# Kernel tuning notes

Measured on AMD Instinct MI355X. Metric: run time of the kernel, lower is better.

The kernel has to match this reference:

```python
import jax, jax.numpy as jnp
import numpy as np

D_MODEL = 1024
N_HEADS = 16
HEAD_DIM = D_MODEL // N_HEADS


def setup_inputs() -> dict:
    key = jax.random.key(0)
    k1, k2, k3 = jax.random.split(key, 3)
    x = jax.random.normal(k1, (4, 2048, D_MODEL), dtype=jnp.float32)
    # torch nn.Linear(d_model, 3*d_model, bias=False): weight [3C, C], y = x @ W.T
    w_qkv = jax.random.normal(k2, (3 * D_MODEL, D_MODEL), dtype=jnp.float32) * (1.0 / np.sqrt(D_MODEL))
    w_out = jax.random.normal(k3, (D_MODEL, D_MODEL), dtype=jnp.float32) * (1.0 / np.sqrt(D_MODEL))
    return {"x": x, "w_qkv": w_qkv, "w_out": w_out}


def reference(x, w_qkv, w_out):
    B, T, C = x.shape
    H, Dh = N_HEADS, HEAD_DIM
    scale = 1.0 / np.sqrt(Dh).astype(np.float32)
    qkv = x @ w_qkv.T  # [B, T, 3C]
    q, k, v = jnp.split(qkv, 3, axis=-1)

    def heads(t):  # [B,T,C] -> [B,H,T,Dh]
        return t.reshape(B, T, H, Dh).transpose(0, 2, 1, 3)

    q, k, v = heads(q), heads(k), heads(v)
    attn = jnp.einsum('bhqd,bhkd->bhqk', q, k) * scale  # [B,H,T,T]
    attn = jax.nn.softmax(attn, axis=-1)
    out = jnp.einsum('bhqk,bhkd->bhqd', attn, v)  # [B,H,T,Dh]
    out = out.transpose(0, 2, 1, 3).reshape(B, T, C)
    return out @ w_out.T
```

## Files before the change

### kernel.cpp

```cpp
#include <hip/hip_runtime.h>
#include <hip/hip_bf16.h>

#define DEVINL __device__ __forceinline__

typedef short s16x8 __attribute__((ext_vector_type(8)));
typedef float f32x4 __attribute__((ext_vector_type(4)));

static constexpr int TC = 1024;
static constexpr int NH = 16;
static constexpr int DH = 64;
static constexpr int TT = 2048;
static constexpr int NB = 4;
static constexpr int MROWS = NB * TT;

static constexpr float QSCALE = 0.18033688011112042f;

DEVINL ushort f32_to_bf16u(float f) {
  uint u = __builtin_bit_cast(uint, f);
  u += 0x7fffu + ((u >> 16) & 1u);
  return (ushort)(u >> 16);
}

DEVINL f32x4 mfma32(s16x8 a, s16x8 b, f32x4 c) {
  return __builtin_amdgcn_mfma_f32_16x16x32_bf16(a, b, c, 0, 0, 0);
}

DEVINL void gload_lds16(const void* g, void* l) {
  __builtin_amdgcn_global_load_lds((const __attribute__((address_space(1))) void*)g,
                                   (__attribute__((address_space(3))) void*)l, 16, 0, 0);
}

DEVINL s16x8 ld8(const ushort* p) { return *reinterpret_cast<const s16x8*>(p); }

DEVINL void cvt_range(const float* __restrict__ src, ushort* __restrict__ dst, int n4,
                      int i0, int stride) {
  for (int i = i0; i < n4; i += stride) {
    float4 v = reinterpret_cast<const float4*>(src)[i];
    ushort4 o;
    o.x = f32_to_bf16u(v.x);
    o.y = f32_to_bf16u(v.y);
    o.z = f32_to_bf16u(v.z);
    o.w = f32_to_bf16u(v.w);
    reinterpret_cast<ushort4*>(dst)[i] = o;
  }
}

__global__ void cvt3_kernel(const float* __restrict__ s0, ushort* __restrict__ d0, int n0,
                            const float* __restrict__ s1, ushort* __restrict__ d1, int n1,
                            const float* __restrict__ s2, ushort* __restrict__ d2, int n2) {
  const int i0 = blockIdx.x * blockDim.x + threadIdx.x;
  const int stride = gridDim.x * blockDim.x;
  cvt_range(s0, d0, n0, i0, stride);
  cvt_range(s1, d1, n1, i0, stride);
  cvt_range(s2, d2, n2, i0, stride);
}

template <int MODE>
__global__ __launch_bounds__(256, 2) void gemm_bt(
    const ushort* __restrict__ A, const ushort* __restrict__ Bw, float* __restrict__ Cout,
    ushort* __restrict__ Qo, ushort* __restrict__ Ko, ushort* __restrict__ Vo, int N) {
  __shared__ __align__(16) ushort As[128 * 64];
  __shared__ __align__(16) ushort Bs[128 * 64];
  const int lane = threadIdx.x & 63;
  const int wid = threadIdx.x >> 6;
  const int bx = blockIdx.x, by = blockIdx.y;
  const int wrow = (wid >> 1) * 64, wcol = (wid & 1) * 64;
  const int lr = lane >> 3;
  const int lc = lane & 7;

  f32x4 acc[4][4] = {};

  for (int kt = 0; kt < TC; kt += 64) {
#pragma unroll
    for (int j = 0; j < 4; ++j) {
      const int seg = wid * 4 + j;
      const int r = seg * 8 + lr;
      const int csrc = lc ^ (r & 7);
      const ushort* ga = A + (size_t)(by * 128 + r) * TC + kt + csrc * 8;
      gload_lds16(ga, &As[seg * 512]);
      const ushort* gb = Bw + (size_t)(bx * 128 + r) * TC + kt + csrc * 8;
      gload_lds16(gb, &Bs[seg * 512]);
    }
    __syncthreads();
#pragma unroll
    for (int kk = 0; kk < 2; ++kk) {
      s16x8 af[4], bfr[4];
#pragma unroll
      for (int m = 0; m < 4; ++m) {
        const int r = wrow + m * 16 + (lane & 15);
        const int ch = (kk * 4 + (lane >> 4)) ^ (r & 7);
        af[m] = *reinterpret_cast<const s16x8*>(&As[r * 64 + ch * 8]);
      }
#pragma unroll
      for (int n = 0; n < 4; ++n) {
        const int r = wcol + n * 16 + (lane & 15);
        const int ch = (kk * 4 + (lane >> 4)) ^ (r & 7);
        bfr[n] = *reinterpret_cast<const s16x8*>(&Bs[r * 64 + ch * 8]);
      }
#pragma unroll
      for (int m = 0; m < 4; ++m)
#pragma unroll
        for (int n = 0; n < 4; ++n) acc[m][n] = mfma32(af[m], bfr[n], acc[m][n]);
    }
    __syncthreads();
  }

#pragma unroll
  for (int m = 0; m < 4; ++m) {
#pragma unroll
    for (int n = 0; n < 4; ++n) {
      const int ng = bx * 128 + wcol + n * 16 + (lane & 15);
      const int mg0 = by * 128 + wrow + m * 16 + (lane >> 4) * 4;
      if (MODE == 0) {
#pragma unroll
        for (int i = 0; i < 4; ++i) Cout[(size_t)(mg0 + i) * N + ng] = acc[m][n][i];
      } else {
        const int sec = ng >> 10;
        const int w = ng & 1023;
        const int h = w >> 6, d = w & 63;
#pragma unroll
        for (int i = 0; i < 4; ++i) {
          const int mg = mg0 + i;
          const int t = mg & (TT - 1);
          const int b = mg >> 11;
          const int bh = b * NH + h;
          const float v = acc[m][n][i];
          if (sec == 0)
            Qo[((size_t)bh * TT + t) * DH + d] = f32_to_bf16u(v * QSCALE);
          else if (sec == 1)
            Ko[((size_t)bh * TT + t) * DH + d] = f32_to_bf16u(v);
          else
            Vo[((size_t)bh * DH + d) * TT + t] = f32_to_bf16u(v);
        }
      }
    }
  }
}

__global__ __launch_bounds__(256, 4) void attn_kernel(const ushort* __restrict__ Q,
                                                      const ushort* __restrict__ K,
                                                      const ushort* __restrict__ V,
                                                      ushort* __restrict__ O) {
  __shared__ __align__(16) ushort Ks[2][64 * 64];
  __shared__ __align__(16) ushort Vs[2][64 * 64];
  const int tid = threadIdx.x;
  const int lane = tid & 63, wid = tid >> 6;
  const int bh = blockIdx.x;
  const int q0 = blockIdx.y * 128 + wid * 32;
  const int qr = lane & 15, lg = lane >> 4;

  const ushort* Qh = Q + (size_t)bh * TT * DH;
  const ushort* Kh = K + (size_t)bh * TT * DH;
  const ushort* Vh = V + (size_t)bh * DH * TT;

  s16x8 qf[2][2];
#pragma unroll
  for (int qt = 0; qt < 2; ++qt)
#pragma unroll
    for (int h = 0; h < 2; ++h)
      qf[qt][h] = ld8(&Qh[(q0 + qt * 16 + qr) * DH + h * 32 + lg * 8]);

  const int pk = 8 * (qr >> 2) + (qr & 3);

  const uint one_bf = 0x3F803F80u;
  const s16x8 ONES = __builtin_bit_cast(s16x8, (uint4){one_bf, one_bf, one_bf, one_bf});

  f32x4 acc[2][4] = {};
  f32x4 acc1[2] = {};

#define SWZ(r) ((r ^ ((r & 8) >> 1)) & 7)

#define STAGE(buf, k0)                                                              \
  {                                                                                 \
    _Pragma("unroll") for (int j = 0; j < 2; ++j) {                                 \
      const int l = tid + 256 * j;                                                  \
      const int row = l >> 3, ch = l & 7;                                           \
      const int sc = ch ^ SWZ(row);                                                 \
      gload_lds16(&Kh[(size_t)((k0) + row) * DH + sc * 8],                          \
                  &Ks[buf][(wid * 64 + 256 * j) * 8]);                              \
      gload_lds16(&Vh[(size_t)row * TT + (k0) + sc * 8],                            \
                  &Vs[buf][(wid * 64 + 256 * j) * 8]);                              \
    }                                                                               \
  }

  STAGE(0, 0);
  __syncthreads();

  for (int t = 0; t < TT / 64; ++t) {
    const int buf = t & 1;
    if (t + 1 < TT / 64) STAGE(buf ^ 1, (t + 1) * 64);
    const ushort* Kb = Ks[buf];
    const ushort* Vb = Vs[buf];

#pragma unroll
    for (int kh = 0; kh < 2; ++kh) {
      s16x8 kf[2][2];
#pragma unroll
      for (int jj = 0; jj < 2; ++jj)
#pragma unroll
        for (int h = 0; h < 2; ++h) {
          const int r = kh * 32 + pk + 4 * jj;
          const int ch = (h * 4 + lg) ^ SWZ(r);
          kf[jj][h] = ld8(&Kb[r * 64 + ch * 8]);
        }
      s16x8 vf[4];
#pragma unroll
      for (int g = 0; g < 4; ++g) {
        const int r = g * 16 + qr;
        const int ch = (kh * 4 + lg) ^ SWZ(r);
        vf[g] = ld8(&Vb[r * 64 + ch * 8]);
      }

#pragma unroll
      for (int qt = 0; qt < 2; ++qt) {
        const f32x4 z = {};
        f32x4 slo = mfma32(kf[0][0], qf[qt][0], z);
        slo = mfma32(kf[0][1], qf[qt][1], slo);
        f32x4 shi = mfma32(kf[1][0], qf[qt][0], z);
        shi = mfma32(kf[1][1], qf[qt][1], shi);

        float p[8];
#pragma unroll
        for (int i = 0; i < 4; ++i) {
          p[i] = __builtin_amdgcn_exp2f(slo[i]);
          p[4 + i] = __builtin_amdgcn_exp2f(shi[i]);
        }

        uint u[4];
#pragma unroll
        for (int e = 0; e < 4; ++e) {
          const uint a0 = __builtin_bit_cast(uint, p[2 * e]) + 0x8000u;
          const uint a1 = __builtin_bit_cast(uint, p[2 * e + 1]) + 0x8000u;
          u[e] = __builtin_amdgcn_perm(a1, a0, 0x07060302u);
        }
        const s16x8 pa = __builtin_bit_cast(s16x8, u);

#pragma unroll
        for (int g = 0; g < 4; ++g) acc[qt][g] = mfma32(pa, vf[g], acc[qt][g]);
        acc1[qt] = mfma32(pa, ONES, acc1[qt]);
      }
    }
    __syncthreads();
  }

  const int b = bh >> 4, h = bh & 15;
#pragma unroll
  for (int qt = 0; qt < 2; ++qt) {
    float inv[4];
#pragma unroll
    for (int i = 0; i < 4; ++i) inv[i] = 1.0f / acc1[qt][i];
#pragma unroll
    for (int g = 0; g < 4; ++g) {
#pragma unroll
      for (int i = 0; i < 4; ++i) {
        const int tq = q0 + qt * 16 + lg * 4 + i;
        const int col = h * DH + g * 16 + qr;
        O[((size_t)b * TT + tq) * TC + col] = f32_to_bf16u(acc[qt][g][i] * inv[i]);
      }
    }
  }
#undef STAGE
#undef SWZ
}

extern "C" void kernel_launch(void* const* d_in, const int* in_sizes, int n_in,
                              void* d_out, int out_size, void* d_ws, size_t ws_size,
                              hipStream_t stream) {
  const float* x = (const float*)d_in[0];
  const float* wqkv = (const float*)d_in[1];
  const float* wout = (const float*)d_in[2];
  float* out = (float*)d_out;
  char* ws = (char*)d_ws;

  ushort* xb    = (ushort*)(ws);
  ushort* wqkvb = (ushort*)(ws + ((size_t)16 << 20));
  ushort* woutb = (ushort*)(ws + ((size_t)22 << 20));
  ushort* qb    = (ushort*)(ws + ((size_t)24 << 20));
  ushort* kb    = (ushort*)(ws + ((size_t)40 << 20));
  ushort* vtb   = (ushort*)(ws + ((size_t)56 << 20));

  cvt3_kernel<<<2048, 256, 0, stream>>>(x, xb, MROWS * TC / 4,
                                        wqkv, wqkvb, 3 * TC * TC / 4,
                                        wout, woutb, TC * TC / 4);

  gemm_bt<1><<<dim3(3 * TC / 128, MROWS / 128), 256, 0, stream>>>(
      xb, wqkvb, nullptr, qb, kb, vtb, 3 * TC);

  attn_kernel<<<dim3(NB * NH, TT / 128), 256, 0, stream>>>(qb, kb, vtb, xb);

  gemm_bt<0><<<dim3(TC / 128, MROWS / 128), 256, 0, stream>>>(
      xb, woutb, out, nullptr, nullptr, nullptr, TC);
}
```

Before: 195.0 us.

## Double-buffer GEMM LDS tiles, swizzle block order, precompute attention LDS offsets

The projection GEMM now double-buffers its A/B shared-memory tiles, so the next K slice loads while MFMAs run on the current one. It also remaps workgroup IDs in an 8-way interleave to improve L2 locality. The attention kernel precomputes its swizzled LDS offsets outside the loop and wraps its MFMA groups in s_setprio to favour matrix issue. Doubling LDS to 64KB per GEMM block may limit the two-blocks-per-CU occupancy the launch bounds request.

```diff
diff --git a/kernel.cpp b/kernel.cpp
--- a/kernel.cpp
+++ b/kernel.cpp
@@ -59,29 +59,43 @@
 __global__ __launch_bounds__(256, 2) void gemm_bt(
     const ushort* __restrict__ A, const ushort* __restrict__ Bw, float* __restrict__ Cout,
     ushort* __restrict__ Qo, ushort* __restrict__ Ko, ushort* __restrict__ Vo, int N) {
-  __shared__ __align__(16) ushort As[128 * 64];
-  __shared__ __align__(16) ushort Bs[128 * 64];
+  __shared__ __align__(16) ushort As[2][128 * 64];
+  __shared__ __align__(16) ushort Bs[2][128 * 64];
   const int lane = threadIdx.x & 63;
   const int wid = threadIdx.x >> 6;
-  const int bx = blockIdx.x, by = blockIdx.y;
+
+  const int nx = gridDim.x;
+  const int nwg = nx * gridDim.y;
+  const int orig = blockIdx.x + nx * blockIdx.y;
+  const int cpx = nwg >> 3;
+  const int swz = (orig & 7) * cpx + (orig >> 3);
+  const int bx = swz % nx, by = swz / nx;
+
   const int wrow = (wid >> 1) * 64, wcol = (wid & 1) * 64;
   const int lr = lane >> 3;
   const int lc = lane & 7;
 
   f32x4 acc[4][4] = {};
 
-  for (int kt = 0; kt < TC; kt += 64) {
-#pragma unroll
-    for (int j = 0; j < 4; ++j) {
-      const int seg = wid * 4 + j;
-      const int r = seg * 8 + lr;
-      const int csrc = lc ^ (r & 7);
-      const ushort* ga = A + (size_t)(by * 128 + r) * TC + kt + csrc * 8;
-      gload_lds16(ga, &As[seg * 512]);
-      const ushort* gb = Bw + (size_t)(bx * 128 + r) * TC + kt + csrc * 8;
-      gload_lds16(gb, &Bs[seg * 512]);
-    }
-    __syncthreads();
+#define GSTAGE(buf, kt)                                                         \
+  {                                                                             \
+    _Pragma("unroll") for (int j = 0; j < 4; ++j) {                             \
+      const int seg = wid * 4 + j;                                              \
+      const int r = seg * 8 + lr;                                               \
+      const int csrc = lc ^ (r & 7);                                            \
+      gload_lds16(A + (size_t)(by * 128 + r) * TC + (kt) + csrc * 8,            \
+                  &As[buf][seg * 512]);                                         \
+      gload_lds16(Bw + (size_t)(bx * 128 + r) * TC + (kt) + csrc * 8,           \
+                  &Bs[buf][seg * 512]);                                         \
+    }                                                                           \
+  }
+
+  GSTAGE(0, 0);
+  __syncthreads();
+
+  for (int t = 0; t < TC / 64; ++t) {
+    const int buf = t & 1;
+    if (t + 1 < TC / 64) GSTAGE(buf ^ 1, (t + 1) * 64);
 #pragma unroll
     for (int kk = 0; kk < 2; ++kk) {
       s16x8 af[4], bfr[4];
@@ -89,13 +103,13 @@
       for (int m = 0; m < 4; ++m) {
         const int r = wrow + m * 16 + (lane & 15);
         const int ch = (kk * 4 + (lane >> 4)) ^ (r & 7);
-        af[m] = *reinterpret_cast<const s16x8*>(&As[r * 64 + ch * 8]);
+        af[m] = ld8(&As[buf][r * 64 + ch * 8]);
       }
 #pragma unroll
       for (int n = 0; n < 4; ++n) {
         const int r = wcol + n * 16 + (lane & 15);
         const int ch = (kk * 4 + (lane >> 4)) ^ (r & 7);
-        bfr[n] = *reinterpret_cast<const s16x8*>(&Bs[r * 64 + ch * 8]);
+        bfr[n] = ld8(&Bs[buf][r * 64 + ch * 8]);
       }
 #pragma unroll
       for (int m = 0; m < 4; ++m)
@@ -104,6 +118,7 @@
     }
     __syncthreads();
   }
+#undef GSTAGE
 
 #pragma unroll
   for (int m = 0; m < 4; ++m) {
@@ -170,6 +185,23 @@
 
 #define SWZ(r) ((r ^ ((r & 8) >> 1)) & 7)
 
+  int koff[2][2][2], voff[2][4];
+#pragma unroll
+  for (int kh = 0; kh < 2; ++kh) {
+#pragma unroll
+    for (int jj = 0; jj < 2; ++jj)
+#pragma unroll
+      for (int h = 0; h < 2; ++h) {
+        const int r = kh * 32 + pk + 4 * jj;
+        koff[kh][jj][h] = r * 64 + ((h * 4 + lg) ^ SWZ(r)) * 8;
+      }
+#pragma unroll
+    for (int g = 0; g < 4; ++g) {
+      const int r = g * 16 + qr;
+      voff[kh][g] = r * 64 + ((kh * 4 + lg) ^ SWZ(r)) * 8;
+    }
+  }
+
 #define STAGE(buf, k0)                                                              \
   {                                                                                 \
     _Pragma("unroll") for (int j = 0; j < 2; ++j) {                                 \
@@ -198,26 +230,20 @@
 #pragma unroll
       for (int jj = 0; jj < 2; ++jj)
 #pragma unroll
-        for (int h = 0; h < 2; ++h) {
-          const int r = kh * 32 + pk + 4 * jj;
-          const int ch = (h * 4 + lg) ^ SWZ(r);
-          kf[jj][h] = ld8(&Kb[r * 64 + ch * 8]);
-        }
+        for (int h = 0; h < 2; ++h) kf[jj][h] = ld8(&Kb[koff[kh][jj][h]]);
       s16x8 vf[4];
 #pragma unroll
-      for (int g = 0; g < 4; ++g) {
-        const int r = g * 16 + qr;
-        const int ch = (kh * 4 + lg) ^ SWZ(r);
-        vf[g] = ld8(&Vb[r * 64 + ch * 8]);
-      }
+      for (int g = 0; g < 4; ++g) vf[g] = ld8(&Vb[voff[kh][g]]);
 
 #pragma unroll
       for (int qt = 0; qt < 2; ++qt) {
         const f32x4 z = {};
+        __builtin_amdgcn_s_setprio(1);
         f32x4 slo = mfma32(kf[0][0], qf[qt][0], z);
         slo = mfma32(kf[0][1], qf[qt][1], slo);
         f32x4 shi = mfma32(kf[1][0], qf[qt][0], z);
         shi = mfma32(kf[1][1], qf[qt][1], shi);
+        __builtin_amdgcn_s_setprio(0);
 
         float p[8];
 #pragma unroll
@@ -235,9 +261,11 @@
         }
         const s16x8 pa = __builtin_bit_cast(s16x8, u);
 
+        __builtin_amdgcn_s_setprio(1);
 #pragma unroll
         for (int g = 0; g < 4; ++g) acc[qt][g] = mfma32(pa, vf[g], acc[qt][g]);
         acc1[qt] = mfma32(pa, ONES, acc1[qt]);
+        __builtin_amdgcn_s_setprio(0);
       }
     }
     __syncthreads();
```

Measured after the change: 196.7 us. About the same (+0.9%).
